# Kernel optimization log

Hardware: AMD Instinct MI355X
Metric: run time of the kernel (lower is better)

## Reference

```python
import jax, jax.numpy as jnp
import numpy as np


def setup_inputs() -> dict:
    key = jax.random.key(0)
    k1, k2 = jax.random.split(key)
    N, D, O, K = 65536, 256, 256, 8  # tokens, inputdim, outdim, degree+1
    gridsize = 8
    x = jax.random.normal(k1, (N, D), dtype=jnp.float32)
    # init stddev = 1/(sqrt(inputdim)*sqrt(gridsize)) as in the module
    std = 1.0 / (np.sqrt(D) * np.sqrt(gridsize))
    cheby_coeffs = jax.random.normal(k2, (O, D, K), dtype=jnp.float32) * std
    bias = jnp.zeros((1, O), dtype=jnp.float32)
    return {"x": x, "cheby_coeffs": cheby_coeffs, "bias": bias}


def reference(x, cheby_coeffs, bias):
    # x: (N, D); cheby_coeffs: (O, D, K); bias: (1, O)
    K = cheby_coeffs.shape[-1]
    xt = jnp.tanh(x)                       # squash into [-1, 1]
    theta = jnp.arccos(xt)                 # (N, D)
    n = jnp.arange(K, dtype=x.dtype)       # Chebyshev orders 0..degree
    # T_n(xt) = cos(n * arccos(xt)), matching the original per-degree loop
    T = jnp.cos(theta[..., None] * n)      # (N, D, K)
    y = jnp.einsum('ndk,odk->no', T, cheby_coeffs)  # (N, O)
    y = y + bias
    return y
```

## Files before the change

kernel.cpp:

```cpp
#include <hip/hip_runtime.h>
#include <hip/hip_bf16.h>

typedef __attribute__((ext_vector_type(4)))  int   i32x4;
typedef __attribute__((ext_vector_type(16))) int   i32x16;

#define DIM_D 256
#define DIM_O 256
#define DIM_K 8
#define BM 128
#define NCHUNK 16
#define NSTEP 4
#define MAGIC 12582912.f

__global__ __launch_bounds__(256) void pack_w_kernel(
    const float* __restrict__ coeffs,
    unsigned int* __restrict__ wp,
    float* __restrict__ scales)
{
    const int o = blockIdx.x;
    const int d = threadIdx.x;
    const float* cp = coeffs + ((size_t)o * DIM_D + d) * DIM_K;
    float4 c0 = *(const float4*)cp;
    float4 c1 = *(const float4*)(cp + 4);

    float m = fmaxf(fmaxf(fmaxf(fabsf(c0.x), fabsf(c0.y)),
                          fmaxf(fabsf(c0.z), fabsf(c0.w))),
                    fmaxf(fmaxf(fabsf(c1.x), fabsf(c1.y)),
                          fmaxf(fabsf(c1.z), fabsf(c1.w))));
    #pragma unroll
    for (int i = 32; i >= 1; i >>= 1)
        m = fmaxf(m, __shfl_xor(m, i));
    __shared__ float wm[4];
    if ((d & 63) == 0) wm[d >> 6] = m;
    __syncthreads();
    const float sc = fmaxf(fmaxf(fmaxf(wm[0], wm[1]), fmaxf(wm[2], wm[3])),
                           1e-30f);
    if (d == 0) scales[o] = sc;

    const float inv = 127.0f / sc;
    unsigned f0 = __float_as_uint(__builtin_fmaf(c0.x, inv, MAGIC));
    unsigned f1 = __float_as_uint(__builtin_fmaf(c0.y, inv, MAGIC));
    unsigned f2 = __float_as_uint(__builtin_fmaf(c0.z, inv, MAGIC));
    unsigned f3 = __float_as_uint(__builtin_fmaf(c0.w, inv, MAGIC));
    unsigned f4 = __float_as_uint(__builtin_fmaf(c1.x, inv, MAGIC));
    unsigned f5 = __float_as_uint(__builtin_fmaf(c1.y, inv, MAGIC));
    unsigned f6 = __float_as_uint(__builtin_fmaf(c1.z, inv, MAGIC));
    unsigned f7 = __float_as_uint(__builtin_fmaf(c1.w, inv, MAGIC));
    unsigned rA = __builtin_amdgcn_perm(f1, f0, 0x00000400u);
    unsigned rB = __builtin_amdgcn_perm(f3, f2, 0x00000400u);
    unsigned rC = __builtin_amdgcn_perm(f5, f4, 0x00000400u);
    unsigned rD = __builtin_amdgcn_perm(f7, f6, 0x00000400u);
    unsigned lo = __builtin_amdgcn_perm(rB, rA, 0x05040100u);
    unsigned hi = __builtin_amdgcn_perm(rD, rC, 0x05040100u);

    const int base = (((d >> 2) * 8 + (o >> 5)) * 64
                      + ((d >> 1) & 1) * 32 + (o & 31)) * 4 + (d & 1) * 2;
    wp[base]     = lo;
    wp[base + 1] = hi;
}

__device__ __forceinline__ void cheb_q8(float xs, unsigned int* o2) {
    float e2 = __expf(2.f * xs);
    float r  = __builtin_amdgcn_rcpf(e2 + 1.f);
    float T1 = __builtin_fmaf(-2.f, r, 1.f);
    float tx = T1 + T1;
    float T2 = __builtin_fmaf(tx, T1, -1.f);
    float T3 = __builtin_fmaf(tx, T2, -T1);
    float T4 = __builtin_fmaf(tx, T3, -T2);
    float T5 = __builtin_fmaf(tx, T4, -T3);
    float T6 = __builtin_fmaf(tx, T5, -T4);
    float T7 = __builtin_fmaf(tx, T6, -T5);
    unsigned f1 = __float_as_uint(__builtin_fmaf(T1, 127.f, MAGIC));
    unsigned f2 = __float_as_uint(__builtin_fmaf(T2, 127.f, MAGIC));
    unsigned f3 = __float_as_uint(__builtin_fmaf(T3, 127.f, MAGIC));
    unsigned f4 = __float_as_uint(__builtin_fmaf(T4, 127.f, MAGIC));
    unsigned f5 = __float_as_uint(__builtin_fmaf(T5, 127.f, MAGIC));
    unsigned f6 = __float_as_uint(__builtin_fmaf(T6, 127.f, MAGIC));
    unsigned f7 = __float_as_uint(__builtin_fmaf(T7, 127.f, MAGIC));
    unsigned rA = __builtin_amdgcn_perm(f2, f1, 0x00000400u);
    unsigned rC = __builtin_amdgcn_perm(f5, f4, 0x00000400u);
    unsigned rD = __builtin_amdgcn_perm(f7, f6, 0x00000400u);
    o2[0] = __builtin_amdgcn_perm(f3, rA, 0x0401000Cu) | 127u;
    o2[1] = __builtin_amdgcn_perm(rD, rC, 0x05040100u);
}

__global__ __launch_bounds__(256, 2) void cfkan_kernel(
    const float* __restrict__ x,
    const i32x4* __restrict__ wp8,
    const float* __restrict__ scales,
    const float* __restrict__ bias,
    float* __restrict__ y)
{
    __shared__ unsigned char Abuf[2][BM][128];

    const int t = threadIdx.x;
    const int w = t >> 6;
    const int l = t & 63;
    const int m = l & 31;
    const int h = l >> 5;
    const int bid = (int)blockIdx.x;
    const int cpx = (int)gridDim.x >> 3;
    const int row0 = ((bid & 7) * cpx + (bid >> 3)) * BM;
    const int ph = bid & 15;

    i32x16 acc[4][2];
    #pragma unroll
    for (int rt = 0; rt < 4; ++rt)
        #pragma unroll
        for (int ct = 0; ct < 2; ++ct)
            #pragma unroll
            for (int qi = 0; qi < 16; ++qi)
                acc[rt][ct][qi] = 0;

    const int lrow = t >> 1;
    const int half = t & 1;
    const float* xrow = x + (size_t)(row0 + lrow) * DIM_D + half * 8;

#define READA(DST, AB, S) do {                                             \
    const int _so = (((2 * (S) + h) ^ (m & 7)) * 16);                      \
    DST[0] = *(const i32x4*)&AB[      m][_so];                             \
    DST[1] = *(const i32x4*)&AB[ 32 + m][_so];                             \
    DST[2] = *(const i32x4*)&AB[ 64 + m][_so];                             \
    DST[3] = *(const i32x4*)&AB[ 96 + m][_so];                             \
} while (0)
#define LOADB2(DST, SG) do {                                               \
    DST[0] = wp8[((SG) * 8 + w * 2 + 0) * 64 + l];                         \
    DST[1] = wp8[((SG) * 8 + w * 2 + 1) * 64 + l];                         \
} while (0)
#define STAGE2(ANX, S, X0, X1) do {                                        \
    union { unsigned int u[4]; i32x4 v; } _tv;                             \
    cheb_q8(X0, &_tv.u[0]);                                                \
    cheb_q8(X1, &_tv.u[2]);                                                \
    *(i32x4*)&ANX[lrow][(((half * 4 + (S)) ^ (lrow & 7)) * 16)] = _tv.v;   \
} while (0)
#define SOFT_BARRIER() do {                                                \
    asm volatile("s_waitcnt lgkmcnt(0)" ::: "memory");                     \
    __builtin_amdgcn_s_barrier();                                          \
    __builtin_amdgcn_sched_barrier(0);                                     \
} while (0)
#define STEP(CUR, NXT, S, DO_READ) do {                                    \
    const int _tgt = ((S) < 2) ? (cc4 + (S) + 2) : (nc4 + (S) - 2);        \
    LOADB2(bq[(S) + 2], _tgt);                                             \
    if (DO_READ) READA(NXT, A, (S) + 1);                                   \
    __builtin_amdgcn_s_setprio(1);                                         \
    _Pragma("unroll")                                                      \
    for (int _rt = 0; _rt < 4; ++_rt) {                                    \
        acc[_rt][0] = __builtin_amdgcn_mfma_i32_32x32x32_i8(               \
            CUR[_rt], bq[S][0], acc[_rt][0], 0, 0, 0);                     \
        acc[_rt][1] = __builtin_amdgcn_mfma_i32_32x32x32_i8(               \
            CUR[_rt], bq[S][1], acc[_rt][1], 0, 0, 0);                     \
    }                                                                      \
    __builtin_amdgcn_s_setprio(0);                                         \
    if (stage) STAGE2(ANX, S, xv[2 * (S)], xv[2 * (S) + 1]);               \
} while (0)

    float xv[8];
    {
        float4 a0 = *(const float4*)(xrow + ph * 16);
        float4 a1 = *(const float4*)(xrow + ph * 16 + 4);
        float xs[8] = {a0.x, a0.y, a0.z, a0.w, a1.x, a1.y, a1.z, a1.w};
        #pragma unroll
        for (int s = 0; s < 4; ++s)
            STAGE2(Abuf[0], s, xs[2 * s], xs[2 * s + 1]);
        const int c1 = (ph + 1) & 15;
        float4 b0 = *(const float4*)(xrow + c1 * 16);
        float4 b1 = *(const float4*)(xrow + c1 * 16 + 4);
        xv[0] = b0.x; xv[1] = b0.y; xv[2] = b0.z; xv[3] = b0.w;
        xv[4] = b1.x; xv[5] = b1.y; xv[6] = b1.z; xv[7] = b1.w;
    }
    i32x4 bq[NSTEP + 2][2];
    LOADB2(bq[0], ph * 4);
    LOADB2(bq[1], ph * 4 + 1);
    SOFT_BARRIER();
    i32x4 ra[4], rb[4];
    READA(ra, Abuf[0], 0);

    #pragma unroll 1
    for (int ci = 0; ci < NCHUNK; ++ci) {
        const int cc  = (ci + ph) & 15;
        const int ncc = (ci + 1 + ph) & 15;
        const unsigned char (*A)[128] = Abuf[ci & 1];
        unsigned char (*ANX)[128]     = Abuf[(ci & 1) ^ 1];
        const bool stage = (ci < NCHUNK - 1);
        float4 xn0, xn1;
        if (ci + 2 < NCHUNK) {
            const int c2 = (ci + 2 + ph) & 15;
            xn0 = *(const float4*)(xrow + c2 * 16);
            xn1 = *(const float4*)(xrow + c2 * 16 + 4);
        }
        const int cc4 = cc * 4, nc4 = ncc * 4;

        STEP(ra, rb, 0, true);
        STEP(rb, ra, 1, true);
        STEP(ra, rb, 2, true);
        STEP(rb, ra, 3, false);

        bq[0][0] = bq[4][0]; bq[0][1] = bq[4][1];
        bq[1][0] = bq[5][0]; bq[1][1] = bq[5][1];
        if (ci + 2 < NCHUNK) {
            xv[0] = xn0.x; xv[1] = xn0.y; xv[2] = xn0.z; xv[3] = xn0.w;
            xv[4] = xn1.x; xv[5] = xn1.y; xv[6] = xn1.z; xv[7] = xn1.w;
        }
        SOFT_BARRIER();
        if (ci < NCHUNK - 1) READA(ra, ANX, 0);
    }

    #pragma unroll
    for (int ct = 0; ct < 2; ++ct) {
        const int col = w * 64 + ct * 32 + m;
        const float sf = scales[col] * (1.f / 16129.f);
        const float bv = bias[col];
        #pragma unroll
        for (int rt = 0; rt < 4; ++rt) {
            #pragma unroll
            for (int qi = 0; qi < 16; ++qi) {
                const int grow = row0 + rt * 32 + (qi & 3) + 8 * (qi >> 2) + 4 * h;
                y[(size_t)grow * DIM_O + col] =
                    __builtin_fmaf((float)acc[rt][ct][qi], sf, bv);
            }
        }
    }
#undef READA
#undef LOADB2
#undef STAGE2
#undef SOFT_BARRIER
#undef STEP
}

extern "C" void kernel_launch(void* const* d_in, const int* in_sizes, int n_in,
                              void* d_out, int out_size, void* d_ws, size_t ws_size,
                              hipStream_t stream) {
    const float* x      = (const float*)d_in[0];
    const float* coeffs = (const float*)d_in[1];
    const float* bias   = (const float*)d_in[2];
    float* y = (float*)d_out;
    float*        scales = (float*)d_ws;
    unsigned int* wp     = (unsigned int*)((char*)d_ws + 1024);

    const int n_tokens = in_sizes[0] / DIM_D;

    pack_w_kernel<<<DIM_O, 256, 0, stream>>>(coeffs, wp, scales);
    cfkan_kernel<<<n_tokens / BM, 256, 0, stream>>>(
        x, (const i32x4*)wp, scales, bias, y);
}
```

Baseline: 53.62 us.

## Split block into producer and consumer warps for Chebyshev staging and MFMA

Doubles the block to 512 threads. Four warps now only compute the Chebyshev int8 quantization and write the A tile into LDS, and the other four only issue the int8 MFMAs and load the weights. The goal is to overlap the transcendental staging work with matrix math across separate waves instead of interleaving both in the same instruction stream. The cost is more waves per block and more register pressure under launch_bounds(512,2), which may reduce occupancy or force spills, and both groups still synchronize at a barrier every chunk.

```diff
diff --git a/kernel.cpp b/kernel.cpp
--- a/kernel.cpp
+++ b/kernel.cpp
@@ -84,7 +84,7 @@
     o2[1] = __builtin_amdgcn_perm(rD, rC, 0x05040100u);
 }
 
-__global__ __launch_bounds__(256, 2) void cfkan_kernel(
+__global__ __launch_bounds__(512, 2) void cfkan_kernel(
     const float* __restrict__ x,
     const i32x4* __restrict__ wp8,
     const float* __restrict__ scales,
@@ -94,7 +94,8 @@
     __shared__ unsigned char Abuf[2][BM][128];
 
     const int t = threadIdx.x;
-    const int w = t >> 6;
+    const int wid = t >> 6;
+    const bool cons = (wid < 4);
     const int l = t & 63;
     const int m = l & 31;
     const int h = l >> 5;
@@ -104,17 +105,14 @@
     const int ph = bid & 15;
 
     i32x16 acc[4][2];
-    #pragma unroll
-    for (int rt = 0; rt < 4; ++rt)
-        #pragma unroll
-        for (int ct = 0; ct < 2; ++ct)
-            #pragma unroll
-            for (int qi = 0; qi < 16; ++qi)
-                acc[rt][ct][qi] = 0;
-
-    const int lrow = t >> 1;
-    const int half = t & 1;
+    i32x4 bq[NSTEP + 2][2];
+    i32x4 ra[4], rb[4];
+
+    const int pt   = t & 255;
+    const int lrow = pt >> 1;
+    const int half = pt & 1;
     const float* xrow = x + (size_t)(row0 + lrow) * DIM_D + half * 8;
+    float xv[8];
 
 #define READA(DST, AB, S) do {                                             \
     const int _so = (((2 * (S) + h) ^ (m & 7)) * 16);                      \
@@ -124,8 +122,8 @@
     DST[3] = *(const i32x4*)&AB[ 96 + m][_so];                             \
 } while (0)
 #define LOADB2(DST, SG) do {                                               \
-    DST[0] = wp8[((SG) * 8 + w * 2 + 0) * 64 + l];                         \
-    DST[1] = wp8[((SG) * 8 + w * 2 + 1) * 64 + l];                         \
+    DST[0] = wp8[((SG) * 8 + wid * 2 + 0) * 64 + l];                       \
+    DST[1] = wp8[((SG) * 8 + wid * 2 + 1) * 64 + l];                       \
 } while (0)
 #define STAGE2(ANX, S, X0, X1) do {                                        \
     union { unsigned int u[4]; i32x4 v; } _tv;                             \
@@ -138,7 +136,7 @@
     __builtin_amdgcn_s_barrier();                                          \
     __builtin_amdgcn_sched_barrier(0);                                     \
 } while (0)
-#define STEP(CUR, NXT, S, DO_READ) do {                                    \
+#define STEPC(CUR, NXT, S, DO_READ) do {                                   \
     const int _tgt = ((S) < 2) ? (cc4 + (S) + 2) : (nc4 + (S) - 2);        \
     LOADB2(bq[(S) + 2], _tgt);                                             \
     if (DO_READ) READA(NXT, A, (S) + 1);                                   \
@@ -151,11 +149,19 @@
             CUR[_rt], bq[S][1], acc[_rt][1], 0, 0, 0);                     \
     }                                                                      \
     __builtin_amdgcn_s_setprio(0);                                         \
-    if (stage) STAGE2(ANX, S, xv[2 * (S)], xv[2 * (S) + 1]);               \
-} while (0)
-
-    float xv[8];
-    {
+} while (0)
+
+    if (cons) {
+        #pragma unroll
+        for (int rt = 0; rt < 4; ++rt)
+            #pragma unroll
+            for (int ct = 0; ct < 2; ++ct)
+                #pragma unroll
+                for (int qi = 0; qi < 16; ++qi)
+                    acc[rt][ct][qi] = 0;
+        LOADB2(bq[0], ph * 4);
+        LOADB2(bq[1], ph * 4 + 1);
+    } else {
         float4 a0 = *(const float4*)(xrow + ph * 16);
         float4 a1 = *(const float4*)(xrow + ph * 16 + 4);
         float xs[8] = {a0.x, a0.y, a0.z, a0.w, a1.x, a1.y, a1.z, a1.w};
@@ -168,55 +174,62 @@
         xv[0] = b0.x; xv[1] = b0.y; xv[2] = b0.z; xv[3] = b0.w;
         xv[4] = b1.x; xv[5] = b1.y; xv[6] = b1.z; xv[7] = b1.w;
     }
-    i32x4 bq[NSTEP + 2][2];
-    LOADB2(bq[0], ph * 4);
-    LOADB2(bq[1], ph * 4 + 1);
     SOFT_BARRIER();
-    i32x4 ra[4], rb[4];
-    READA(ra, Abuf[0], 0);
+    if (cons) READA(ra, Abuf[0], 0);
 
     #pragma unroll 1
     for (int ci = 0; ci < NCHUNK; ++ci) {
-        const int cc  = (ci + ph) & 15;
-        const int ncc = (ci + 1 + ph) & 15;
         const unsigned char (*A)[128] = Abuf[ci & 1];
         unsigned char (*ANX)[128]     = Abuf[(ci & 1) ^ 1];
-        const bool stage = (ci < NCHUNK - 1);
-        float4 xn0, xn1;
-        if (ci + 2 < NCHUNK) {
-            const int c2 = (ci + 2 + ph) & 15;
-            xn0 = *(const float4*)(xrow + c2 * 16);
-            xn1 = *(const float4*)(xrow + c2 * 16 + 4);
+
+        if (cons) {
+            const int cc  = (ci + ph) & 15;
+            const int ncc = (ci + 1 + ph) & 15;
+            const int cc4 = cc * 4, nc4 = ncc * 4;
+            STEPC(ra, rb, 0, true);
+            STEPC(rb, ra, 1, true);
+            STEPC(ra, rb, 2, true);
+            STEPC(rb, ra, 3, false);
+            bq[0][0] = bq[4][0]; bq[0][1] = bq[4][1];
+            bq[1][0] = bq[5][0]; bq[1][1] = bq[5][1];
+        } else {
+            float4 xn0, xn1;
+            if (ci + 2 < NCHUNK) {
+                const int c2 = (ci + 2 + ph) & 15;
+                xn0 = *(const float4*)(xrow + c2 * 16);
+                xn1 = *(const float4*)(xrow + c2 * 16 + 4);
+            }
+            if (ci < NCHUNK - 1) {
+                STAGE2(ANX, 0, xv[0], xv[1]);
+                STAGE2(ANX, 1, xv[2], xv[3]);
+                STAGE2(ANX, 2, xv[4], xv[5]);
+                STAGE2(ANX, 3, xv[6], xv[7]);
+            }
+            if (ci + 2 < NCHUNK) {
+                xv[0] = xn0.x; xv[1] = xn0.y; xv[2] = xn0.z; xv[3] = xn0.w;
+                xv[4] = xn1.x; xv[5] = xn1.y; xv[6] = xn1.z; xv[7] = xn1.w;
+            }
         }
-        const int cc4 = cc * 4, nc4 = ncc * 4;
-
-        STEP(ra, rb, 0, true);
-        STEP(rb, ra, 1, true);
-        STEP(ra, rb, 2, true);
-        STEP(rb, ra, 3, false);
-
-        bq[0][0] = bq[4][0]; bq[0][1] = bq[4][1];
-        bq[1][0] = bq[5][0]; bq[1][1] = bq[5][1];
-        if (ci + 2 < NCHUNK) {
-            xv[0] = xn0.x; xv[1] = xn0.y; xv[2] = xn0.z; xv[3] = xn0.w;
-            xv[4] = xn1.x; xv[5] = xn1.y; xv[6] = xn1.z; xv[7] = xn1.w;
-        }
+
         SOFT_BARRIER();
-        if (ci < NCHUNK - 1) READA(ra, ANX, 0);
+        if (cons && ci < NCHUNK - 1) READA(ra, ANX, 0);
     }
 
-    #pragma unroll
-    for (int ct = 0; ct < 2; ++ct) {
-        const int col = w * 64 + ct * 32 + m;
-        const float sf = scales[col] * (1.f / 16129.f);
-        const float bv = bias[col];
+    if (cons) {
         #pragma unroll
-        for (int rt = 0; rt < 4; ++rt) {
+        for (int ct = 0; ct < 2; ++ct) {
+            const int col = wid * 64 + ct * 32 + m;
+            const float sf = scales[col] * (1.f / 16129.f);
+            const float bv = bias[col];
             #pragma unroll
-            for (int qi = 0; qi < 16; ++qi) {
-                const int grow = row0 + rt * 32 + (qi & 3) + 8 * (qi >> 2) + 4 * h;
-                y[(size_t)grow * DIM_O + col] =
-                    __builtin_fmaf((float)acc[rt][ct][qi], sf, bv);
+            for (int rt = 0; rt < 4; ++rt) {
+                #pragma unroll
+                for (int qi = 0; qi < 16; ++qi) {
+                    const int grow = row0 + rt * 32
+                                   + (qi & 3) + 8 * (qi >> 2) + 4 * h;
+                    y[(size_t)grow * DIM_O + col] =
+                        __builtin_fmaf((float)acc[rt][ct][qi], sf, bv);
+                }
             }
         }
     }
@@ -224,7 +237,7 @@
 #undef LOADB2
 #undef STAGE2
 #undef SOFT_BARRIER
-#undef STEP
+#undef STEPC
 }
 
 extern "C" void kernel_launch(void* const* d_in, const int* in_sizes, int n_in,
@@ -240,6 +253,6 @@
     const int n_tokens = in_sizes[0] / DIM_D;
 
     pack_w_kernel<<<DIM_O, 256, 0, stream>>>(coeffs, wp, scales);
-    cfkan_kernel<<<n_tokens / BM, 256, 0, stream>>>(
+    cfkan_kernel<<<n_tokens / BM, 512, 0, stream>>>(
         x, (const i32x4*)wp, scales, bias, y);
 }
```

New measurement: 60.04 us. +12.0%, slower.
